# Kernel optimization log

Hardware: AMD Instinct MI355X
Metric: run time of the kernel (lower is better)

The kernel has to match this reference:

```python
import jax, jax.numpy as jnp
import numpy as np

N_VIEWS = 4
VIEW_DIM = 48
N_CLASSES = 16
D = VIEW_DIM ** N_VIEWS  # 5,308,416 cross-feature dims


def setup_inputs() -> dict:
    key = jax.random.key(0)
    kx, kw = jax.random.split(key)
    x = jax.random.normal(kx, (N_VIEWS, VIEW_DIM), dtype=jnp.float32)
    # pyg Linear(-1, n_classes): kaiming_uniform weight (scale ~ 1/sqrt(fan_in)), zero bias
    W = jax.random.normal(kw, (N_CLASSES, D), dtype=jnp.float32) * np.float32(1.0 / np.sqrt(D))
    b = jnp.zeros((N_CLASSES,), dtype=jnp.float32)
    return {"x": x, "W": W, "b": b}


def _cross_feature_tensor(x):
    # Faithful to construct_cross_feature_discovery_tensor:
    # outer(x0, x1) -> flatten -> outer(., x2) -> flatten -> ...
    # Loop is over the fixed, small n_views axis (static under jit).
    t = jnp.outer(x[0], x[1]).ravel()          # (VIEW_DIM**2,)
    for v in x[2:]:
        t = jnp.outer(t, v).ravel()            # grows to VIEW_DIM**k
    return t                                   # (D,)


def reference(x, W, b):
    cfdt = _cross_feature_tensor(x)            # (D,)
    return jax.nn.relu(W @ cfdt + b)           # (N_CLASSES,)
```

## Files before the change

### kernel.cpp

```cpp
#include <hip/hip_runtime.h>


#define N_CLASSES 16
#define VIEW_DIM  48
#define P         2304
#define D         5308416
#define CHUNKS    256
#define BLOCK     256

__global__ void vcdn_zero_ws(float* ws) {
    if (threadIdx.x < N_CLASSES) ws[threadIdx.x] = 0.0f;
}

__global__ __launch_bounds__(BLOCK) void vcdn_main(
        const float* __restrict__ x,
        const float* __restrict__ W,
        float* __restrict__ ws) {
    __shared__ float p01[P];
    __shared__ float p23[P];

    const float* x0 = x;
    const float* x1 = x + VIEW_DIM;
    const float* x2 = x + 2 * VIEW_DIM;
    const float* x3 = x + 3 * VIEW_DIM;

    for (int t = threadIdx.x; t < P; t += BLOCK) {
        int i = t / VIEW_DIM;
        int j = t - i * VIEW_DIM;
        p01[t] = x0[i] * x1[j];
        p23[t] = x2[i] * x3[j];
    }
    __syncthreads();

    const int c     = blockIdx.x / CHUNKS;
    const int chunk = blockIdx.x - c * CHUNKS;

    const float4* W4 = (const float4*)(W + (size_t)c * D);
    const float4* q4 = (const float4*)p23;

    const int nvec   = D / 4;
    const int stride = CHUNKS * BLOCK;

    float acc = 0.0f;
    for (int v = chunk * BLOCK + threadIdx.x; v < nvec; v += stride) {
        int d    = v << 2;
        int a    = d / P;
        int bidx = d - a * P;
        float4 w = W4[v];
        float4 q = q4[bidx >> 2];
        acc += p01[a] * (w.x * q.x + w.y * q.y + w.z * q.z + w.w * q.w);
    }

    for (int off = 32; off > 0; off >>= 1)
        acc += __shfl_down(acc, off, 64);

    __shared__ float wsum[BLOCK / 64];
    const int lane = threadIdx.x & 63;
    const int wid  = threadIdx.x >> 6;
    if (lane == 0) wsum[wid] = acc;
    __syncthreads();
    if (threadIdx.x == 0) {
        float s = wsum[0] + wsum[1] + wsum[2] + wsum[3];
        atomicAdd(&ws[c], s);
    }
}

__global__ void vcdn_finalize(const float* __restrict__ ws,
                              const float* __restrict__ b,
                              float* __restrict__ out) {
    int c = threadIdx.x;
    if (c < N_CLASSES) {
        float v = ws[c] + b[c];
        out[c] = v > 0.0f ? v : 0.0f;
    }
}

extern "C" void kernel_launch(void* const* d_in, const int* in_sizes, int n_in,
                              void* d_out, int out_size, void* d_ws, size_t ws_size,
                              hipStream_t stream) {
    const float* x = (const float*)d_in[0];
    const float* W = (const float*)d_in[1];
    const float* b = (const float*)d_in[2];
    float* out = (float*)d_out;
    float* ws  = (float*)d_ws;

    vcdn_zero_ws<<<1, 64, 0, stream>>>(ws);
    vcdn_main<<<N_CLASSES * CHUNKS, BLOCK, 0, stream>>>(x, W, ws);
    vcdn_finalize<<<1, 64, 0, stream>>>(ws, b, out);
}
```

Baseline: 461.7 us.

## Restructure GEMV so each wave handles whole rows with register-cached p23

The cross-feature dot product is reorganised so each wave processes complete P-length rows of W, holding the p23 outer-product slice in registers and computing one p01 scalar per row. This removes the per-element integer division and shared-memory gathers of the grid-stride loop. Atomics and the zeroing kernel are replaced by per-block partial sums, which a wider finalize kernel reduces in a fixed order. The cost is a higher register footprint from the cached q values and a larger grid of blocks.

```diff
diff --git a/kernel.cpp b/kernel.cpp
--- a/kernel.cpp
+++ b/kernel.cpp
@@ -4,19 +4,17 @@
 #define N_CLASSES 16
 #define VIEW_DIM  48
 #define P         2304
-#define D         5308416
-#define CHUNKS    256
+#define ROW_F4    (P / 4)
+#define CHUNKS    288
+#define ROWS_PER_BLOCK 8
+#define ROWS_PER_WAVE  2
 #define BLOCK     256
-
-__global__ void vcdn_zero_ws(float* ws) {
-    if (threadIdx.x < N_CLASSES) ws[threadIdx.x] = 0.0f;
-}
+#define ITERS     (ROW_F4 / 64)
 
 __global__ __launch_bounds__(BLOCK) void vcdn_main(
         const float* __restrict__ x,
         const float* __restrict__ W,
         float* __restrict__ ws) {
-    __shared__ float p01[P];
     __shared__ float p23[P];
 
     const float* x0 = x;
@@ -27,51 +25,70 @@
     for (int t = threadIdx.x; t < P; t += BLOCK) {
         int i = t / VIEW_DIM;
         int j = t - i * VIEW_DIM;
-        p01[t] = x0[i] * x1[j];
         p23[t] = x2[i] * x3[j];
     }
     __syncthreads();
 
     const int c     = blockIdx.x / CHUNKS;
     const int chunk = blockIdx.x - c * CHUNKS;
+    const int wid   = threadIdx.x >> 6;
+    const int lane  = threadIdx.x & 63;
 
-    const float4* W4 = (const float4*)(W + (size_t)c * D);
     const float4* q4 = (const float4*)p23;
+    float4 q[ITERS];
+#pragma unroll
+    for (int it = 0; it < ITERS; ++it) q[it] = q4[it * 64 + lane];
 
-    const int nvec   = D / 4;
-    const int stride = CHUNKS * BLOCK;
+    const int row0 = chunk * ROWS_PER_BLOCK + wid * ROWS_PER_WAVE;
+    float acc = 0.0f;
 
-    float acc = 0.0f;
-    for (int v = chunk * BLOCK + threadIdx.x; v < nvec; v += stride) {
-        int d    = v << 2;
-        int a    = d / P;
-        int bidx = d - a * P;
-        float4 w = W4[v];
-        float4 q = q4[bidx >> 2];
-        acc += p01[a] * (w.x * q.x + w.y * q.y + w.z * q.z + w.w * q.w);
+#pragma unroll
+    for (int r = 0; r < ROWS_PER_WAVE; ++r) {
+        const int a = row0 + r;
+        const int i = a / VIEW_DIM;
+        const int j = a - i * VIEW_DIM;
+        const float s01 = x0[i] * x1[j];
+
+        const float4* Wrow =
+            (const float4*)(W + (size_t)c * (size_t)P * P + (size_t)a * P);
+
+        float racc = 0.0f;
+#pragma unroll
+        for (int it = 0; it < ITERS; ++it) {
+            float4 w = Wrow[it * 64 + lane];
+            racc += w.x * q[it].x + w.y * q[it].y + w.z * q[it].z + w.w * q[it].w;
+        }
+        acc += s01 * racc;
     }
 
-    for (int off = 32; off > 0; off >>= 1)
+    for (int off = 32; off; off >>= 1)
         acc += __shfl_down(acc, off, 64);
 
     __shared__ float wsum[BLOCK / 64];
-    const int lane = threadIdx.x & 63;
-    const int wid  = threadIdx.x >> 6;
     if (lane == 0) wsum[wid] = acc;
     __syncthreads();
-    if (threadIdx.x == 0) {
-        float s = wsum[0] + wsum[1] + wsum[2] + wsum[3];
-        atomicAdd(&ws[c], s);
-    }
+    if (threadIdx.x == 0)
+        ws[c * CHUNKS + chunk] = wsum[0] + wsum[1] + wsum[2] + wsum[3];
 }
 
 __global__ void vcdn_finalize(const float* __restrict__ ws,
                               const float* __restrict__ b,
                               float* __restrict__ out) {
-    int c = threadIdx.x;
-    if (c < N_CLASSES) {
-        float v = ws[c] + b[c];
-        out[c] = v > 0.0f ? v : 0.0f;
+    __shared__ float s[BLOCK];
+    const int t   = threadIdx.x;
+    const int c   = t >> 4;
+    const int sub = t & 15;
+    float sum = 0.0f;
+    for (int k = sub; k < CHUNKS; k += 16)
+        sum += ws[c * CHUNKS + k];
+    s[t] = sum;
+    __syncthreads();
+    if (t < N_CLASSES) {
+        float tot = 0.0f;
+#pragma unroll
+        for (int k = 0; k < 16; ++k) tot += s[t * 16 + k];
+        tot += b[t];
+        out[t] = tot > 0.0f ? tot : 0.0f;
     }
 }
 
@@ -84,7 +101,6 @@
     float* out = (float*)d_out;
     float* ws  = (float*)d_ws;
 
-    vcdn_zero_ws<<<1, 64, 0, stream>>>(ws);
     vcdn_main<<<N_CLASSES * CHUNKS, BLOCK, 0, stream>>>(x, W, ws);
-    vcdn_finalize<<<1, 64, 0, stream>>>(ws, b, out);
+    vcdn_finalize<<<1, BLOCK, 0, stream>>>(ws, b, out);
 }
```

After: 449.4 us. -2.7%, faster.
